# Kernel optimization log

Measured on AMD Instinct MI355X. Metric: run time of the kernel, lower is better.

## Reference

```python
import jax, jax.numpy as jnp
import numpy as np

IN_DIM = 4096
OUT_DIM = 2048
K = 4
R = 4096
B = 4096


def setup_inputs() -> dict:
    key = jax.random.key(0)
    ks = jax.random.split(key, 8)
    s = 0.02
    return {
        "hidden_states": jax.random.normal(ks[0], (B, IN_DIM), jnp.float32),
        # stacked per-block weights, torch Linear layout: W1/W3 [k+1, out, in], W2 [k+1, in, out]
        "W1": jax.random.normal(ks[1], (K + 1, OUT_DIM, IN_DIM), jnp.float32) * s,
        "W3": jax.random.normal(ks[2], (K + 1, OUT_DIM, IN_DIM), jnp.float32) * s,
        "W2": jax.random.normal(ks[3], (K + 1, IN_DIM, OUT_DIM), jnp.float32) * s,
        "fc1_w": jax.random.normal(ks[4], (R, IN_DIM * K), jnp.float32) * s,
        "fc1_b": jax.random.normal(ks[5], (R,), jnp.float32) * s,
        "fc2_w": jax.random.normal(ks[6], (IN_DIM, R), jnp.float32) * s,
        "fc2_b": jax.random.normal(ks[7], (IN_DIM,), jnp.float32) * s,
    }


def reference(hidden_states, W1, W3, W2, fc1_w, fc1_b, fc2_w, fc2_b):
    x = hidden_states
    # batched SwiGLU over k+1 blocks: [B, k+1, out]
    g = jax.nn.silu(jnp.einsum("bi,koi->bko", x, W1)) * jnp.einsum("bi,koi->bko", x, W3)
    wk_outs = jnp.einsum("bko,kio->bki", g, W2)  # [B, k+1, in]
    o0 = wk_outs[:, 0]                            # [B, in]
    concat = wk_outs[:, 1:].reshape(x.shape[0], -1)  # [B, k*in], matches torch.cat order
    h = jax.nn.silu(concat @ fc1_w.T + fc1_b)
    proj = h @ fc2_w.T + fc2_b                    # [B, in]
    diff = o0 - proj
    return (jnp.linalg.norm(diff, ord=2, axis=1), jnp.mean(jnp.abs(diff), axis=1))
```

## Files before the change

kernel.cpp:

```cpp
#include <hip/hip_runtime.h>
#include <hip/hip_bf16.h>
#include <cstdint>
#include <cstddef>

#define IN_DIM 4096
#define OUT_DIM 2048
#define NEXP 5
#define KEXP 4
#define RDIM 4096
#define BATCH 4096

typedef __hip_bfloat16 bf16;
typedef __attribute__((ext_vector_type(8))) short bf16x8;
typedef __attribute__((ext_vector_type(4))) float f32x4;
typedef __attribute__((ext_vector_type(8))) unsigned short u16x8;

typedef const __attribute__((address_space(1))) unsigned int* as1p;
typedef __attribute__((address_space(3))) unsigned int* as3p;

__device__ __forceinline__ unsigned short f2bf(float x) {
  union { __hip_bfloat16 h; unsigned short u; } cv;
  cv.h = __float2bfloat16(x);
  return cv.u;
}

__global__ __launch_bounds__(256) void cvt_kernel(const float* __restrict__ in,
                                                  unsigned short* __restrict__ out,
                                                  int n8) {
  int i = blockIdx.x * 256 + threadIdx.x;
  if (i >= n8) return;
  const float4* p = (const float4*)in;
  float4 a = p[(size_t)i * 2];
  float4 b = p[(size_t)i * 2 + 1];
  u16x8 v;
  v[0] = f2bf(a.x); v[1] = f2bf(a.y); v[2] = f2bf(a.z); v[3] = f2bf(a.w);
  v[4] = f2bf(b.x); v[5] = f2bf(b.y); v[6] = f2bf(b.z); v[7] = f2bf(b.w);
  *(u16x8*)(out + (size_t)i * 8) = v;
}

__device__ __forceinline__ void gload16(const bf16* g, bf16* l) {
  __builtin_amdgcn_global_load_lds((as1p)g, (as3p)l, 16, 0, 0);
}

template <int N> __device__ __forceinline__ void vwait() {
  if constexpr (N == 0) asm volatile("s_waitcnt vmcnt(0)" ::: "memory");
  else if constexpr (N == 2) asm volatile("s_waitcnt vmcnt(2)" ::: "memory");
  else if constexpr (N == 4) asm volatile("s_waitcnt vmcnt(4)" ::: "memory");
}

#define READ_A(buf, mh)                                              \
  do {                                                               \
    const bf16* _pa = ldsA + (buf) * 16384 + (mh) * 8192;            \
    _Pragma("unroll") for (int m2 = 0; m2 < 4; ++m2) {               \
      afr[m2][0] = *(const bf16x8*)(_pa + aOff[m2]);                 \
      afr[m2][1] = *(const bf16x8*)(_pa + (aOff[m2] ^ 32));          \
    }                                                                \
  } while (0)

#define READ_B(buf, nh)                                              \
  do {                                                               \
    const bf16* _pb = ldsB + (buf) * 16384 + (nh) * 8192;            \
    _Pragma("unroll") for (int n2 = 0; n2 < 2; ++n2) {               \
      bfr[(nh) * 2 + n2][0] = *(const bf16x8*)(_pb + bOff[(nh) * 2 + n2]);        \
      bfr[(nh) * 2 + n2][1] = *(const bf16x8*)(_pb + (bOff[(nh) * 2 + n2] ^ 32)); \
    }                                                                \
  } while (0)

#define QMFMA(mh, nh)                                                            \
  do {                                                                           \
    __builtin_amdgcn_s_setprio(1);                                               \
    _Pragma("unroll") for (int m2 = 0; m2 < 4; ++m2) {                           \
      _Pragma("unroll") for (int n2 = 0; n2 < 2; ++n2) {                         \
        acc[(mh) * 4 + m2][(nh) * 2 + n2] = __builtin_amdgcn_mfma_f32_16x16x32_bf16( \
            afr[m2][0], bfr[(nh) * 2 + n2][0], acc[(mh) * 4 + m2][(nh) * 2 + n2], 0, 0, 0); \
        acc[(mh) * 4 + m2][(nh) * 2 + n2] = __builtin_amdgcn_mfma_f32_16x16x32_bf16( \
            afr[m2][1], bfr[(nh) * 2 + n2][1], acc[(mh) * 4 + m2][(nh) * 2 + n2], 0, 0, 0); \
      }                                                                          \
    }                                                                            \
    __builtin_amdgcn_s_setprio(0);                                               \
  } while (0)

#define BAR() __builtin_amdgcn_s_barrier()

template <int EPI>
__global__ __launch_bounds__(512, 2) void gemm8p(
    const bf16* __restrict__ A, int lda, long long aZ,
    const bf16* __restrict__ B, int ldb, long long bZ,
    int Kdim,
    unsigned short* __restrict__ C, int ldc, long long cZ,
    const float* __restrict__ bias,
    const bf16* __restrict__ AUX, int ldaux, long long auxZ,
    float* __restrict__ accum,
    int gx, int gxy, int nwg8) {
  extern __shared__ __align__(16) bf16 lds[];
  bf16* ldsA = lds;
  bf16* ldsB = lds + 32768;

  int flat = blockIdx.x;
  int wg = (flat & 7) * nwg8 + (flat >> 3);
  int z = wg / gxy;
  int r0 = wg - z * gxy;
  int by = r0 / gx;
  int bx = r0 - by * gx;
  int rowBase = by * 256, colBase = bx * 256;

  int tid = threadIdx.x;
  int wave = tid >> 6, lane = tid & 63;
  int wr = wave >> 2, wc = wave & 3;

  const bf16* Ab = A + (long long)z * aZ + (long long)rowBase * lda;
  const bf16* Bb = B + (long long)z * bZ + (long long)colBase * ldb;

  int rl = tid >> 3;
  int cg8 = ((tid & 7) ^ (rl & 7)) << 3;
  int srcA = rl * lda + cg8;
  int srcB = rl * ldb + cg8;
  int dstOfs = wave * 512;

  int aOff[4], bOff[4];
#pragma unroll
  for (int m2 = 0; m2 < 4; ++m2) {
    int rA = ((2 * m2 + wr) * 16) + (lane & 15);
    aOff[m2] = rA * 64 + (((lane >> 4) ^ (rA & 7)) << 3);
  }
#pragma unroll
  for (int n = 0; n < 4; ++n) {
    int rB = (((4 * n + wc) * 16) & 127) + (lane & 15);
    bOff[n] = rB * 64 + (((lane >> 4) ^ (rB & 7)) << 3);
  }

  f32x4 acc[8][4] = {};
  bf16x8 afr[4][2], bfr[4][2];

  auto stA = [&](int buf, int hh, int kt) {
    const bf16* s = Ab + (long long)(hh * 128) * lda + kt * 64;
    bf16* d = ldsA + buf * 16384 + hh * 8192 + dstOfs;
    gload16(s + srcA, d);
    gload16(s + srcA + 64 * lda, d + 4096);
  };
  auto stB = [&](int buf, int hh, int kt) {
    const bf16* s = Bb + (long long)(hh * 128) * ldb + kt * 64;
    bf16* d = ldsB + buf * 16384 + hh * 8192 + dstOfs;
    gload16(s + srcB, d);
    gload16(s + srcB + 64 * ldb, d + 4096);
  };

  int NT = Kdim >> 6;
  int cur = 0;

  stA(0, 0, 0); stB(0, 0, 0); stB(0, 1, 0); stA(0, 1, 0);
  vwait<4>();
  BAR();

  for (int t = 0; t < NT - 1; ++t) {
    int nb = cur ^ 1;
    READ_A(cur, 0);
    READ_B(cur, 0);
    stA(nb, 0, t + 1);
    vwait<4>();
    BAR();
    QMFMA(0, 0);
    READ_B(cur, 1);
    stB(nb, 0, t + 1);
    vwait<4>();
    BAR();
    QMFMA(0, 1);
    READ_A(cur, 1);
    stB(nb, 1, t + 1);
    BAR();
    QMFMA(1, 1);
    stA(nb, 1, t + 1);
    vwait<4>();
    BAR();
    QMFMA(1, 0);
    cur = nb;
  }

  READ_A(cur, 0);
  READ_B(cur, 0);
  vwait<2>();
  BAR();
  QMFMA(0, 0);
  READ_B(cur, 1);
  vwait<0>();
  BAR();
  QMFMA(0, 1);
  READ_A(cur, 1);
  QMFMA(1, 1);
  QMFMA(1, 0);

  if constexpr (EPI == 2) {
    const bf16* AUXb = AUX + (long long)z * auxZ;
#pragma unroll
    for (int m = 0; m < 8; ++m) {
#pragma unroll
      for (int r = 0; r < 4; ++r) {
        int row = rowBase + (2 * m + wr) * 16 + ((lane >> 4) << 2) + r;
        float ssq = 0.f, sab = 0.f;
#pragma unroll
        for (int n = 0; n < 4; ++n) {
          int col = colBase + (4 * n + wc) * 16 + (lane & 15);
          float p = acc[m][n][r] + bias[col];
          float d = __bfloat162float(AUXb[(long long)row * ldaux + col]) - p;
          ssq += d * d;
          sab += fabsf(d);
        }
#pragma unroll
        for (int off = 1; off < 16; off <<= 1) {
          ssq += __shfl_xor(ssq, off);
          sab += __shfl_xor(sab, off);
        }
        if ((lane & 15) == 0) {
          atomicAdd(&accum[row], ssq);
          atomicAdd(&accum[BATCH + row], sab);
        }
      }
    }
  } else {
    unsigned short* Cb = C + (long long)z * cZ;
    const bf16* AUXb = (EPI == 3) ? (AUX + (long long)z * auxZ) : nullptr;
#pragma unroll
    for (int m = 0; m < 8; ++m) {
#pragma unroll
      for (int n = 0; n < 4; ++n) {
        int col = colBase + (4 * n + wc) * 16 + (lane & 15);
#pragma unroll
        for (int r = 0; r < 4; ++r) {
          int row = rowBase + (2 * m + wr) * 16 + ((lane >> 4) << 2) + r;
          float v = acc[m][n][r];
          if constexpr (EPI == 1) {
            v += bias[col];
            v = v / (1.f + __expf(-v));
          } else if constexpr (EPI == 3) {
            float s = __bfloat162float(AUXb[(long long)row * ldaux + col]);
            v = v * (s / (1.f + __expf(-s)));
          }
          Cb[(long long)row * ldc + col] = f2bf(v);
        }
      }
    }
  }
}

__global__ void zero_accum(float* a) {
  int i = blockIdx.x * 256 + threadIdx.x;
  if (i < 2 * BATCH) a[i] = 0.f;
}

__global__ void finalize_kernel(const float* __restrict__ accum, float* __restrict__ out) {
  int b = blockIdx.x * 256 + threadIdx.x;
  if (b < BATCH) {
    out[b] = sqrtf(accum[b]);
    out[BATCH + b] = accum[BATCH + b] * (1.f / IN_DIM);
  }
}

extern "C" void kernel_launch(void* const* d_in, const int* in_sizes, int n_in,
                              void* d_out, int out_size, void* d_ws, size_t ws_size,
                              hipStream_t stream) {
  const float* x    = (const float*)d_in[0];
  const float* W1   = (const float*)d_in[1];
  const float* W3   = (const float*)d_in[2];
  const float* W2   = (const float*)d_in[3];
  const float* fc1w = (const float*)d_in[4];
  const float* fc1b = (const float*)d_in[5];
  const float* fc2w = (const float*)d_in[6];
  const float* fc2b = (const float*)d_in[7];
  float* out = (float*)d_out;

  char* ws = (char*)d_ws;
  size_t off = 0;
  auto alloc = [&](size_t bytes) {
    char* p = ws + off;
    off += (bytes + 255) & ~(size_t)255;
    return p;
  };
  bf16* xb   = (bf16*)alloc((size_t)BATCH * IN_DIM * 2);
  bf16* w1b  = (bf16*)alloc((size_t)NEXP * OUT_DIM * IN_DIM * 2);
  bf16* w3b  = (bf16*)alloc((size_t)NEXP * OUT_DIM * IN_DIM * 2);
  bf16* w2b  = (bf16*)alloc((size_t)NEXP * IN_DIM * OUT_DIM * 2);
  bf16* f1b  = (bf16*)alloc((size_t)RDIM * IN_DIM * KEXP * 2);
  bf16* f2b  = (bf16*)alloc((size_t)IN_DIM * RDIM * 2);
  bf16* gbuf = (bf16*)alloc((size_t)BATCH * NEXP * OUT_DIM * 2);
  bf16* wk   = (bf16*)alloc((size_t)BATCH * NEXP * IN_DIM * 2);
  bf16* hbuf = (bf16*)alloc((size_t)BATCH * RDIM * 2);
  float* accum = (float*)alloc((size_t)2 * BATCH * 4);
  if (off > ws_size) return;

  bf16* t1 = wk;

  auto cvt = [&](const float* in, bf16* outp, size_t n) {
    int n8 = (int)(n / 8);
    cvt_kernel<<<(n8 + 255) / 256, 256, 0, stream>>>(in, (unsigned short*)outp, n8);
  };
  cvt(x,    xb,  (size_t)BATCH * IN_DIM);
  cvt(W1,   w1b, (size_t)NEXP * OUT_DIM * IN_DIM);
  cvt(W3,   w3b, (size_t)NEXP * OUT_DIM * IN_DIM);
  cvt(W2,   w2b, (size_t)NEXP * IN_DIM * OUT_DIM);
  cvt(fc1w, f1b, (size_t)RDIM * IN_DIM * KEXP);
  cvt(fc2w, f2b, (size_t)IN_DIM * RDIM);

  const size_t LDSB = 131072;

  {
    int gx = OUT_DIM / 256, gxy = gx * (BATCH / 256), nwg = gxy * NEXP;
    gemm8p<0><<<nwg, 512, LDSB, stream>>>(
        xb, IN_DIM, 0LL,
        w1b, IN_DIM, (long long)OUT_DIM * IN_DIM,
        IN_DIM,
        (unsigned short*)t1, NEXP * OUT_DIM, (long long)OUT_DIM,
        nullptr, nullptr, 0, 0LL, nullptr,
        gx, gxy, nwg / 8);
  }
  {
    int gx = OUT_DIM / 256, gxy = gx * (BATCH / 256), nwg = gxy * NEXP;
    gemm8p<3><<<nwg, 512, LDSB, stream>>>(
        xb, IN_DIM, 0LL,
        w3b, IN_DIM, (long long)OUT_DIM * IN_DIM,
        IN_DIM,
        (unsigned short*)gbuf, NEXP * OUT_DIM, (long long)OUT_DIM,
        nullptr, t1, NEXP * OUT_DIM, (long long)OUT_DIM, nullptr,
        gx, gxy, nwg / 8);
  }
  {
    int gx = IN_DIM / 256, gxy = gx * (BATCH / 256), nwg = gxy * NEXP;
    gemm8p<0><<<nwg, 512, LDSB, stream>>>(
        gbuf, NEXP * OUT_DIM, (long long)OUT_DIM,
        w2b, OUT_DIM, (long long)IN_DIM * OUT_DIM,
        OUT_DIM,
        (unsigned short*)wk, NEXP * IN_DIM, (long long)IN_DIM,
        nullptr, nullptr, 0, 0LL, nullptr,
        gx, gxy, nwg / 8);
  }
  {
    int gx = RDIM / 256, gxy = gx * (BATCH / 256), nwg = gxy;
    gemm8p<1><<<nwg, 512, LDSB, stream>>>(
        wk + IN_DIM, NEXP * IN_DIM, 0LL,
        f1b, KEXP * IN_DIM, 0LL,
        KEXP * IN_DIM,
        (unsigned short*)hbuf, RDIM, 0LL,
        fc1b, nullptr, 0, 0LL, nullptr,
        gx, gxy, nwg / 8);
  }
  zero_accum<<<(2 * BATCH + 255) / 256, 256, 0, stream>>>(accum);
  {
    int gx = IN_DIM / 256, gxy = gx * (BATCH / 256), nwg = gxy;
    gemm8p<2><<<nwg, 512, LDSB, stream>>>(
        hbuf, RDIM, 0LL,
        f2b, RDIM, 0LL,
        RDIM,
        nullptr, 0, 0LL,
        fc2b, wk, NEXP * IN_DIM, 0LL, accum,
        gx, gxy, nwg / 8);
  }
  finalize_kernel<<<(BATCH + 255) / 256, 256, 0, stream>>>(accum, out);
}
```

Before: 1.647 ms.

## Fold W2 expert projections into fc1 weights to shrink the fc1 reduction

Instead of computing the four non-zero expert W2 outputs and feeding their concatenation into fc1, the code precomputes Pcat = fc1_w · W2_k per expert (weights-only GEMM) using a transposed bf16 copy of W2. fc1 then contracts directly over the gated activations with reduction length 4*OUT_DIM instead of 4*IN_DIM, and only expert 0 still goes through W2. This drops a large batch-sized GEMM and halves the fc1 reduction, at the cost of an extra weight-weight GEMM, a transpose-convert kernel, and an extra bf16 rounding of the fused weights.

```diff
diff --git a/kernel.cpp b/kernel.cpp
--- a/kernel.cpp
+++ b/kernel.cpp
@@ -14,6 +14,7 @@
 typedef __attribute__((ext_vector_type(8))) short bf16x8;
 typedef __attribute__((ext_vector_type(4))) float f32x4;
 typedef __attribute__((ext_vector_type(8))) unsigned short u16x8;
+typedef __attribute__((ext_vector_type(4))) unsigned short u16x4;
 
 typedef const __attribute__((address_space(1))) unsigned int* as1p;
 typedef __attribute__((address_space(3))) unsigned int* as3p;
@@ -36,6 +37,28 @@
   v[0] = f2bf(a.x); v[1] = f2bf(a.y); v[2] = f2bf(a.z); v[3] = f2bf(a.w);
   v[4] = f2bf(b.x); v[5] = f2bf(b.y); v[6] = f2bf(b.z); v[7] = f2bf(b.w);
   *(u16x8*)(out + (size_t)i * 8) = v;
+}
+
+__global__ __launch_bounds__(256) void tcvt_kernel(const float* __restrict__ in,
+                                                   unsigned short* __restrict__ out,
+                                                   int NI, int NO) {
+  __shared__ float tile[32][33];
+  const float* inz = in + (size_t)blockIdx.z * NI * NO;
+  unsigned short* outz = out + (size_t)blockIdx.z * NI * NO;
+  int i0 = blockIdx.y * 32;
+  int o0 = blockIdx.x * 32;
+  int t = threadIdx.x;
+  int ri = t >> 3, ro = (t & 7) << 2;
+  float4 v = *(const float4*)(inz + (size_t)(i0 + ri) * NO + o0 + ro);
+  tile[ri][ro] = v.x; tile[ri][ro + 1] = v.y; tile[ri][ro + 2] = v.z; tile[ri][ro + 3] = v.w;
+  __syncthreads();
+  int wo = t >> 3, wi = (t & 7) << 2;
+  u16x4 w;
+  w[0] = f2bf(tile[wi][wo]);
+  w[1] = f2bf(tile[wi + 1][wo]);
+  w[2] = f2bf(tile[wi + 2][wo]);
+  w[3] = f2bf(tile[wi + 3][wo]);
+  *(u16x4*)(outz + (size_t)(o0 + wo) * NI + i0 + wi) = w;
 }
 
 __device__ __forceinline__ void gload16(const bf16* g, bf16* l) {
@@ -278,27 +301,31 @@
   bf16* xb   = (bf16*)alloc((size_t)BATCH * IN_DIM * 2);
   bf16* w1b  = (bf16*)alloc((size_t)NEXP * OUT_DIM * IN_DIM * 2);
   bf16* w3b  = (bf16*)alloc((size_t)NEXP * OUT_DIM * IN_DIM * 2);
-  bf16* w2b  = (bf16*)alloc((size_t)NEXP * IN_DIM * OUT_DIM * 2);
+  bf16* w2b0 = (bf16*)alloc((size_t)IN_DIM * OUT_DIM * 2);
+  bf16* w2t  = (bf16*)alloc((size_t)KEXP * OUT_DIM * IN_DIM * 2);
   bf16* f1b  = (bf16*)alloc((size_t)RDIM * IN_DIM * KEXP * 2);
   bf16* f2b  = (bf16*)alloc((size_t)IN_DIM * RDIM * 2);
   bf16* gbuf = (bf16*)alloc((size_t)BATCH * NEXP * OUT_DIM * 2);
-  bf16* wk   = (bf16*)alloc((size_t)BATCH * NEXP * IN_DIM * 2);
+  bf16* t1   = (bf16*)alloc((size_t)BATCH * NEXP * OUT_DIM * 2);
+  bf16* o0   = (bf16*)alloc((size_t)BATCH * IN_DIM * 2);
   bf16* hbuf = (bf16*)alloc((size_t)BATCH * RDIM * 2);
   float* accum = (float*)alloc((size_t)2 * BATCH * 4);
   if (off > ws_size) return;
 
-  bf16* t1 = wk;
+  bf16* Pcat = t1;
 
   auto cvt = [&](const float* in, bf16* outp, size_t n) {
     int n8 = (int)(n / 8);
     cvt_kernel<<<(n8 + 255) / 256, 256, 0, stream>>>(in, (unsigned short*)outp, n8);
   };
-  cvt(x,    xb,  (size_t)BATCH * IN_DIM);
-  cvt(W1,   w1b, (size_t)NEXP * OUT_DIM * IN_DIM);
-  cvt(W3,   w3b, (size_t)NEXP * OUT_DIM * IN_DIM);
-  cvt(W2,   w2b, (size_t)NEXP * IN_DIM * OUT_DIM);
-  cvt(fc1w, f1b, (size_t)RDIM * IN_DIM * KEXP);
-  cvt(fc2w, f2b, (size_t)IN_DIM * RDIM);
+  cvt(x,    xb,   (size_t)BATCH * IN_DIM);
+  cvt(W1,   w1b,  (size_t)NEXP * OUT_DIM * IN_DIM);
+  cvt(W3,   w3b,  (size_t)NEXP * OUT_DIM * IN_DIM);
+  cvt(W2,   w2b0, (size_t)IN_DIM * OUT_DIM);
+  cvt(fc1w, f1b,  (size_t)RDIM * IN_DIM * KEXP);
+  cvt(fc2w, f2b,  (size_t)IN_DIM * RDIM);
+  tcvt_kernel<<<dim3(OUT_DIM / 32, IN_DIM / 32, KEXP), 256, 0, stream>>>(
+      W2 + (size_t)IN_DIM * OUT_DIM, (unsigned short*)w2t, IN_DIM, OUT_DIM);
 
   const size_t LDSB = 131072;
 
@@ -323,21 +350,31 @@
         gx, gxy, nwg / 8);
   }
   {
-    int gx = IN_DIM / 256, gxy = gx * (BATCH / 256), nwg = gxy * NEXP;
+    int gx = IN_DIM / 256, gxy = gx * (BATCH / 256), nwg = gxy;
     gemm8p<0><<<nwg, 512, LDSB, stream>>>(
-        gbuf, NEXP * OUT_DIM, (long long)OUT_DIM,
-        w2b, OUT_DIM, (long long)IN_DIM * OUT_DIM,
+        gbuf, NEXP * OUT_DIM, 0LL,
+        w2b0, OUT_DIM, 0LL,
         OUT_DIM,
-        (unsigned short*)wk, NEXP * IN_DIM, (long long)IN_DIM,
+        (unsigned short*)o0, IN_DIM, 0LL,
+        nullptr, nullptr, 0, 0LL, nullptr,
+        gx, gxy, nwg / 8);
+  }
+  {
+    int gx = OUT_DIM / 256, gxy = gx * (RDIM / 256), nwg = gxy * KEXP;
+    gemm8p<0><<<nwg, 512, LDSB, stream>>>(
+        f1b, KEXP * IN_DIM, (long long)IN_DIM,
+        w2t, IN_DIM, (long long)OUT_DIM * IN_DIM,
+        IN_DIM,
+        (unsigned short*)Pcat, KEXP * OUT_DIM, (long long)OUT_DIM,
         nullptr, nullptr, 0, 0LL, nullptr,
         gx, gxy, nwg / 8);
   }
   {
     int gx = RDIM / 256, gxy = gx * (BATCH / 256), nwg = gxy;
     gemm8p<1><<<nwg, 512, LDSB, stream>>>(
-        wk + IN_DIM, NEXP * IN_DIM, 0LL,
-        f1b, KEXP * IN_DIM, 0LL,
-        KEXP * IN_DIM,
+        gbuf + OUT_DIM, NEXP * OUT_DIM, 0LL,
+        Pcat, KEXP * OUT_DIM, 0LL,
+        KEXP * OUT_DIM,
         (unsigned short*)hbuf, RDIM, 0LL,
         fc1b, nullptr, 0, 0LL, nullptr,
         gx, gxy, nwg / 8);
@@ -350,7 +387,7 @@
         f2b, RDIM, 0LL,
         RDIM,
         nullptr, 0, 0LL,
-        fc2b, wk, NEXP * IN_DIM, 0LL, accum,
+        fc2b, o0, IN_DIM, 0LL, accum,
         gx, gxy, nwg / 8);
   }
   finalize_kernel<<<(BATCH + 255) / 256, 256, 0, stream>>>(accum, out);
```

Result: faster. 1.447 ms (-12.1%).
